# Kernel optimization log

Hardware: AMD Instinct MI355X
Metric: run time of the kernel (lower is better)

Reference implementation:

```python
import jax, jax.numpy as jnp
import numpy as np

B, S, R, D, A, P = 64, 128, 8, 10000, 10, 256


def setup_inputs() -> dict:
    key = jax.random.key(0)
    ks = jax.random.split(key, 7)
    return {
        "atom_hvs": jax.random.normal(ks[0], (A, D), jnp.float32),
        "pos_hvs": jax.random.normal(ks[1], (S, D), jnp.float32),
        "closure_tag": jax.random.normal(ks[2], (D,), jnp.float32),
        "W": jax.random.normal(ks[3], (P, D), jnp.float32) / np.float32(np.sqrt(D)),
        "b": jax.random.normal(ks[4], (P,), jnp.float32) * 0.01,
        "token_mask": jnp.ones((B, S), jnp.float32),
        "ring_mask": jnp.ones((B, R), jnp.float32),
        "atom_idx": jax.random.randint(ks[5], (B, S), 0, A),
        "ring_pos": jax.random.randint(ks[6], (B, R, 2), 0, S),
    }


def reference(atom_hvs, pos_hvs, closure_tag, W, b, token_mask, ring_mask, atom_idx, ring_pos):
    # HRR bind = circular convolution -> pointwise multiply in rFFT domain.
    # Bundle = sum; by linearity we sum in the frequency domain and do a
    # single irfft per molecule (same math as per-token conv + add).
    d = atom_hvs.shape[-1]
    Fa = jnp.fft.rfft(atom_hvs, axis=-1)          # [A, F]
    Fp = jnp.fft.rfft(pos_hvs, axis=-1)           # [S, F]
    Fc = jnp.fft.rfft(closure_tag)                # [F]

    s = atom_idx.shape[1]
    tok = Fa[atom_idx] * Fp[None, :s, :]          # [B, S, F] gather+bind
    freq = jnp.sum(token_mask[..., None] * tok, axis=1)   # [B, F] bundle

    ring = Fp[ring_pos[..., 0]] * Fp[ring_pos[..., 1]] * Fc  # [B, R, F]
    freq = freq + jnp.sum(ring_mask[..., None] * ring, axis=1)

    mol_hv = jnp.fft.irfft(freq, n=d, axis=-1)    # [B, D]
    return mol_hv @ W.T + b                       # [B, proj_dim]
```

## Files before the change

kernel.cpp:

```cpp
#include <hip/hip_runtime.h>

#define PI2 6.28318530717958647692f

#define NSIG 139
#define FS   5120

__global__ __launch_bounds__(256) void k_fwd(
                     const float* __restrict__ atom, const float* __restrict__ pos,
                     const float* __restrict__ clo, float2* __restrict__ spec) {
  __shared__ float xs[4000];
  unsigned sig = blockIdx.x, q = blockIdx.y;
  unsigned k1base = q * 10u;
  unsigned nk1 = (k1base + 10u <= 51u) ? 10u : (51u - k1base);
  const float* xb = (sig < 128u) ? (pos + sig * 10000u)
                   : ((sig < 138u) ? (atom + (sig - 128u) * 10000u) : clo);
  int tid = threadIdx.x;
  unsigned ntile1 = nk1 * 25u;
  unsigned k1l = tid / 25u, n2 = (tid % 25u) * 4u;
  bool have = (unsigned)tid < ntile1;
  unsigned k1 = k1base + k1l;
  float cth, sth;
  __sincosf(PI2 * (float)k1 * 0.01f, &sth, &cth);
  float c = 1.0f, s = 0.0f;
  float ar[4] = {}, as[4] = {};

  if (have) {
#pragma unroll 10
    for (int n1l = 0; n1l < 100; ++n1l) {
      const float4 xv = *(const float4*)(xb + n1l * 100 + n2);
      ar[0] += xv.x * c; as[0] += xv.x * s;
      ar[1] += xv.y * c; as[1] += xv.y * s;
      ar[2] += xv.z * c; as[2] += xv.z * s;
      ar[3] += xv.w * c; as[3] += xv.w * s;
      float cn = c * cth - s * sth;
      float sn = s * cth + c * sth;
      c = cn; s = sn;
    }
    unsigned rb = (100u - k1) % 100u;
    float resA[8], resB[8];
#pragma unroll
    for (int j = 0; j < 4; ++j) {
      float swA, cwA, swB, cwB;
      __sincosf(PI2 * (float)((n2 + j) * k1) * 1e-4f, &swA, &cwA);
      __sincosf(PI2 * (float)((n2 + j) * rb) * 1e-4f, &swB, &cwB);
      resA[2 * j + 0] = ar[j] * cwA - as[j] * swA;
      resA[2 * j + 1] = -(as[j] * cwA + ar[j] * swA);
      resB[2 * j + 0] = ar[j] * cwB + as[j] * swB;
      resB[2 * j + 1] = as[j] * cwB - ar[j] * swB;
    }
    float* pA = xs + k1l * 200u + n2 * 2u;
    float* pB = xs + (nk1 + k1l) * 200u + n2 * 2u;
    *(float4*)(pA + 0) = make_float4(resA[0], resA[1], resA[2], resA[3]);
    *(float4*)(pA + 4) = make_float4(resA[4], resA[5], resA[6], resA[7]);
    *(float4*)(pB + 0) = make_float4(resB[0], resB[1], resB[2], resB[3]);
    *(float4*)(pB + 4) = make_float4(resB[4], resB[5], resB[6], resB[7]);
  }
  __syncthreads();

  unsigned nrow = 2u * nk1;
  unsigned ntile3 = nrow * 26u;
  for (unsigned t = tid; t < ntile3; t += 256u) {
    unsigned lr = t / 26u, k2 = (t % 26u) * 2u;
    unsigned gk1 = (lr < nk1) ? (k1base + lr) : ((100u - (k1base + (lr - nk1))) % 100u);
    const float* brow = xs + lr * 200u;
    float cthA, sthA, cthB, sthB;
    __sincosf(PI2 * (float)k2 * 0.01f, &sthA, &cthA);
    __sincosf(PI2 * (float)(k2 + 1) * 0.01f, &sthB, &cthB);
    float cA = 1.0f, sA = 0.0f, cB = 1.0f, sB = 0.0f;
    float reA = 0.f, imA = 0.f, reB = 0.f, imB = 0.f;
#pragma unroll 4
    for (int n2i = 0; n2i < 100; n2i += 2) {
      const float4 b0 = *(const float4*)(brow + 2 * n2i);
      reA += b0.x * cA + b0.y * sA;  imA += b0.y * cA - b0.x * sA;
      reB += b0.x * cB + b0.y * sB;  imB += b0.y * cB - b0.x * sB;
      float cA1 = cA * cthA - sA * sthA, sA1 = sA * cthA + cA * sthA;
      float cB1 = cB * cthB - sB * sthB, sB1 = sB * cthB + cB * sthB;
      reA += b0.z * cA1 + b0.w * sA1;  imA += b0.w * cA1 - b0.z * sA1;
      reB += b0.z * cB1 + b0.w * sB1;  imB += b0.w * cB1 - b0.z * sB1;
      cA = cA1 * cthA - sA1 * sthA; sA = sA1 * cthA + cA1 * sthA;
      cB = cB1 * cthB - sB1 * sthB; sB = sB1 * cthB + cB1 * sthB;
    }
    unsigned kA = gk1 + 100u * k2;
    unsigned kB = gk1 + 100u * (k2 + 1);
    if (kA <= 5000u) spec[sig * FS + kA] = make_float2(reA, imA);
    if (kB <= 5000u) spec[sig * FS + kB] = make_float2(reB, imB);
  }
}

__global__ __launch_bounds__(256) void k_mix(const float2* __restrict__ spec,
                      const float* __restrict__ tmask, const float* __restrict__ rmask,
                      const int* __restrict__ aidx, const int* __restrict__ rpos,
                      float2* __restrict__ G) {
  __shared__ float2 FaS[10][128];
  __shared__ float2 FcS[128];
  __shared__ float tmS[4][128];
  __shared__ int   aiS[4][128];
  __shared__ float rmS[4][8];
  __shared__ int   rpS[4][8][2];
  __shared__ float2 red[2][4][128];
  int tid = threadIdx.x;
  int kl = tid & 127, half = tid >> 7;
  int k = blockIdx.x * 128 + kl;
  int kc = k > 5000 ? 5000 : k;
  int b0 = blockIdx.y * 4;
  for (int i = tid; i < 10 * 128; i += 256) {
    int a = i >> 7, kk = i & 127;
    int kg = blockIdx.x * 128 + kk; if (kg > 5000) kg = 5000;
    FaS[a][kk] = spec[(128 + a) * FS + kg];
  }
  if (tid < 128) FcS[tid] = spec[138 * FS + kc];
  for (int i = tid; i < 4 * 128; i += 256) {
    int bb = i >> 7, ss = i & 127;
    tmS[bb][ss] = tmask[(b0 + bb) * 128 + ss];
    aiS[bb][ss] = aidx[(b0 + bb) * 128 + ss];
  }
  if (tid < 32) {
    int bb = tid >> 3, rr = tid & 7;
    rmS[bb][rr] = rmask[(b0 + bb) * 8 + rr];
    rpS[bb][rr][0] = rpos[((b0 + bb) * 8 + rr) * 2 + 0];
    rpS[bb][rr][1] = rpos[((b0 + bb) * 8 + rr) * 2 + 1];
  }
  __syncthreads();
  float fr[4] = {}, fi[4] = {};
  int sbase = half * 64;
#pragma unroll 8
  for (int si = 0; si < 64; ++si) {
    int s = sbase + si;
    float2 fp = spec[s * FS + kc];
#pragma unroll
    for (int b = 0; b < 4; ++b) {
      int a = aiS[b][s];
      float tm = tmS[b][s];
      float2 fa = FaS[a][kl];
      fr[b] += tm * (fa.x * fp.x - fa.y * fp.y);
      fi[b] += tm * (fa.x * fp.y + fa.y * fp.x);
    }
  }
  float2 fc = FcS[kl];
#pragma unroll
  for (int rr = 0; rr < 4; ++rr) {
    int r = half * 4 + rr;
#pragma unroll
    for (int b = 0; b < 4; ++b) {
      int p0 = rpS[b][r][0], p1 = rpS[b][r][1];
      float rm = rmS[b][r];
      float2 f0 = spec[p0 * FS + kc];
      float2 f1 = spec[p1 * FS + kc];
      float tr = f0.x * f1.x - f0.y * f1.y;
      float ti = f0.x * f1.y + f0.y * f1.x;
      fr[b] += rm * (tr * fc.x - ti * fc.y);
      fi[b] += rm * (tr * fc.y + ti * fc.x);
    }
  }
#pragma unroll
  for (int b = 0; b < 4; ++b) red[half][b][kl] = make_float2(fr[b], fi[b]);
  __syncthreads();
  if (k <= 5000) {
#pragma unroll
    for (int j = 0; j < 2; ++j) {
      int b = half + 2 * j;
      float R = red[0][b][kl].x + red[1][b][kl].x;
      float I = red[0][b][kl].y + red[1][b][kl].y;
      if (k == 0 || k == 5000) I = 0.0f;
      G[(size_t)(b0 + b) * 10000 + k] = make_float2(R, I);
      if (k >= 1 && k <= 4999)
        G[(size_t)(b0 + b) * 10000 + (10000 - k)] = make_float2(R, -I);
    }
  }
}

__global__ __launch_bounds__(256) void k_i1(const float2* __restrict__ G,
                                            float2* __restrict__ Bi) {
  unsigned sig = blockIdx.x;
  const float* gp = (const float*)(G + sig * 10000u);
  int tid = threadIdx.x;
  unsigned t = blockIdx.y * 256u + tid;
  if (t >= 2600u) return;
  unsigned m1 = t / 26u, n2 = (t % 26u) * 2u;
  float cth, sth;
  __sincosf(PI2 * (float)m1 * 0.01f, &sth, &cth);
  float reA = 0.f, imA = 0.f, reB = 0.f, imB = 0.f;

  for (int h = 0; h < 4; ++h) {
    unsigned ph = (m1 * (unsigned)h) & 3u;
    float c = (ph == 0u) ? 1.0f : (ph == 2u) ? -1.0f : 0.0f;
    float s = (ph == 1u) ? 1.0f : (ph == 3u) ? -1.0f : 0.0f;
#pragma unroll 5
    for (int n1l = 0; n1l < 25; ++n1l) {
      const float4 gv = *(const float4*)(gp + (h * 25 + n1l) * 200 + n2 * 2);
      reA += gv.x * c - gv.y * s;  imA += gv.y * c + gv.x * s;
      reB += gv.z * c - gv.w * s;  imB += gv.w * c + gv.z * s;
      float cn = c * cth - s * sth;
      float sn = s * cth + c * sth;
      c = cn; s = sn;
    }
  }
  float w0 = (n2 == 0u || n2 == 50u) ? 0.5f : 1.0f;
  float w1 = (n2 == 50u) ? 0.0f : 1.0f;
  float sw0, cw0, sw1, cw1;
  __sincosf(PI2 * (float)(n2 * m1) * 1e-4f, &sw0, &cw0);
  __sincosf(PI2 * (float)((n2 + 1u) * m1) * 1e-4f, &sw1, &cw1);
  float4 outv;
  outv.x = (reA * cw0 - imA * sw0) * w0;
  outv.y = (imA * cw0 + reA * sw0) * w0;
  outv.z = (reB * cw1 - imB * sw1) * w1;
  outv.w = (imB * cw1 + reB * sw1) * w1;
  *(float4*)((float*)Bi + (sig * 5200u + m1 * 52u + n2) * 2) = outv;
}

__global__ __launch_bounds__(256) void k_i2(const float2* __restrict__ Bi,
                                            float* __restrict__ mol) {
  unsigned sig = blockIdx.x, q = blockIdx.y;
  int tid = threadIdx.x;
  unsigned t = blockIdx.z * 256u + tid;
  if (t >= 1250u) return;
  unsigned m1l = t / 50u;
  unsigned m2 = (t % 50u) * 2u;
  const float* b0 = (const float*)Bi + sig * 10400u + q * 2600u + m1l * 104u;
  float cthA, sthA, cthB, sthB;
  __sincosf(PI2 * (float)m2 * 0.01f, &sthA, &cthA);
  __sincosf(PI2 * (float)(m2 + 1u) * 0.01f, &sthB, &cthB);
  float cA = 1.0f, sA = 0.0f, cB = 1.0f, sB = 0.0f;
  float r0 = 0.f, r1 = 0.f;
#pragma unroll 4
  for (int jj = 0; jj < 26; ++jj) {
    int n2i = 2 * jj;
    const float4 v0 = *(const float4*)(b0 + 2 * n2i);
    r0 += v0.x * cA - v0.y * sA;
    r1 += v0.x * cB - v0.y * sB;
    float cA1 = cA * cthA - sA * sthA, sA1 = sA * cthA + cA * sthA;
    float cB1 = cB * cthB - sB * sthB, sB1 = sB * cthB + cB * sthB;
    r0 += v0.z * cA1 - v0.w * sA1;
    r1 += v0.z * cB1 - v0.w * sB1;
    cA = cA1 * cthA - sA1 * sthA; sA = sA1 * cthA + cA1 * sthA;
    cB = cB1 * cthB - sB1 * sthB; sB = sB1 * cthB + cB1 * sthB;
  }
  unsigned m1 = q * 25u + m1l;
  mol[sig * 10000u + m1 + 100u * m2] = r0 * 2e-4f;
  mol[sig * 10000u + m1 + 100u * (m2 + 1u)] = r1 * 2e-4f;
}

__global__ __launch_bounds__(512) void k_proj(const float* __restrict__ mol,
                                              const float* __restrict__ W,
                                              float* __restrict__ part) {
  __shared__ float molS[40 * 66];
  __shared__ float WS[40][258];
  int tid = threadIdx.x;
  int d0 = blockIdx.x * 40;
  for (int i = tid; i < 40 * 64; i += 512) {
    int b = i / 40, dl = i % 40;
    molS[dl * 66 + b] = mol[(size_t)b * 10000 + d0 + dl];
  }
  for (int i = tid; i < 40 * 256; i += 512) {
    int p = i / 40, dl = i % 40;
    WS[dl][p] = W[(size_t)p * 10000 + d0 + dl];
  }
  __syncthreads();
  int p0 = (tid & 127) * 2;
  int bh = (tid >> 7) * 16;
  float acc[2][16] = {};
#pragma unroll 4
  for (int dl = 0; dl < 40; ++dl) {
    const float2 wv = *(const float2*)(&WS[dl][p0]);
    const float2* m2p = (const float2*)(molS + dl * 66 + bh);
#pragma unroll
    for (int qq = 0; qq < 8; ++qq) {
      float2 mv = m2p[qq];
      acc[0][2 * qq + 0] += wv.x * mv.x;  acc[1][2 * qq + 0] += wv.y * mv.x;
      acc[0][2 * qq + 1] += wv.x * mv.y;  acc[1][2 * qq + 1] += wv.y * mv.y;
    }
  }
#pragma unroll
  for (int b = 0; b < 16; ++b)
    *(float2*)(part + (size_t)blockIdx.x * 16384 + (bh + b) * 256 + p0) =
        make_float2(acc[0][b], acc[1][b]);
}

__global__ __launch_bounds__(256) void k_red(const float* __restrict__ part,
                                             const float* __restrict__ bias,
                                             float* __restrict__ out) {
  __shared__ float red[4][64];
  int tid = threadIdx.x;
  int pl = tid & 63, cg = tid >> 6;
  int b = blockIdx.x;
  int p = blockIdx.y * 64 + pl;
  float acc = 0.0f;
#pragma unroll 8
  for (int ch = cg; ch < 250; ch += 4)
    acc += part[(size_t)ch * 16384 + b * 256 + p];
  red[cg][pl] = acc;
  __syncthreads();
  if (tid < 64)
    out[b * 256 + p] = red[0][pl] + red[1][pl] + red[2][pl] + red[3][pl] + bias[p];
}

extern "C" void kernel_launch(void* const* d_in, const int* in_sizes, int n_in,
                              void* d_out, int out_size, void* d_ws, size_t ws_size,
                              hipStream_t stream) {
  const float* atom  = (const float*)d_in[0];
  const float* pos   = (const float*)d_in[1];
  const float* clo   = (const float*)d_in[2];
  const float* W     = (const float*)d_in[3];
  const float* bias  = (const float*)d_in[4];
  const float* tmask = (const float*)d_in[5];
  const float* rmask = (const float*)d_in[6];
  const int*   aidx  = (const int*)d_in[7];
  const int*   rpos  = (const int*)d_in[8];
  float* out = (float*)d_out;

  char* ws = (char*)d_ws;
  size_t off = 0;
  auto alloc = [&](size_t n) { off = (off + 255) & ~(size_t)255; size_t o = off; off += n; return o; };
  char* regA   = ws + alloc(16777216);
  float2* Bi   = (float2*)regA;
  float*  part = (float*)regA;
  float2* spec = (float2*)(ws + alloc((size_t)NSIG * FS * 8));
  float2* G    = (float2*)(ws + alloc((size_t)64 * 10000 * 8));
  float*  mol  = (float*)(ws + alloc((size_t)64 * 10000 * 4));

  k_fwd<<<dim3(NSIG, 6), dim3(256), 0, stream>>>(atom, pos, clo, spec);
  k_mix<<<dim3(40, 16), dim3(256), 0, stream>>>(spec, tmask, rmask, aidx, rpos, G);
  k_i1<<<dim3(64, 11), dim3(256), 0, stream>>>(G, Bi);
  k_i2<<<dim3(64, 4, 5), dim3(256), 0, stream>>>(Bi, mol);
  k_proj<<<dim3(250), dim3(512), 0, stream>>>(mol, W, part);
  k_red<<<dim3(64, 4), dim3(256), 0, stream>>>(part, bias, out);
}
```

Baseline: 185.4 us.

## Apply radix-4 pre-butterflies in LDS to shrink DFT inner loops

In the forward and first inverse DFT stages, inputs are first combined with a radix-4 butterfly: sums and differences of the four quarter-offset elements are staged in shared memory. The per-thread twiddle loops then run over 25 terms instead of 100, picking the precombined arrays by the index modulo 4. The second forward stage gets the same treatment across its 100-point rows. This cuts multiply-adds and global reads, at the cost of extra LDS traffic, extra syncs and a larger shared-memory footprint, which may lower occupancy.

```diff
diff --git a/kernel.cpp b/kernel.cpp
--- a/kernel.cpp
+++ b/kernel.cpp
@@ -8,36 +8,75 @@
 __global__ __launch_bounds__(256) void k_fwd(
                      const float* __restrict__ atom, const float* __restrict__ pos,
                      const float* __restrict__ clo, float2* __restrict__ spec) {
-  __shared__ float xs[4000];
+  __shared__ float lds[10000];
   unsigned sig = blockIdx.x, q = blockIdx.y;
   unsigned k1base = q * 10u;
   unsigned nk1 = (k1base + 10u <= 51u) ? 10u : (51u - k1base);
   const float* xb = (sig < 128u) ? (pos + sig * 10000u)
                    : ((sig < 138u) ? (atom + (sig - 128u) * 10000u) : clo);
   int tid = threadIdx.x;
+
+  {
+    float* csA = lds;
+    float* csB = lds + 2500;
+    float* csG = lds + 5000;
+    float* csH = lds + 7500;
+    for (int t2 = tid; t2 < 625; t2 += 256) {
+      const float* p = xb + (t2 / 25) * 100 + (t2 % 25) * 4;
+      float4 x0 = *(const float4*)(p);
+      float4 x1 = *(const float4*)(p + 2500);
+      float4 x2 = *(const float4*)(p + 5000);
+      float4 x3 = *(const float4*)(p + 7500);
+      float4 A, B, G, H;
+      A.x = (x0.x + x2.x) + (x1.x + x3.x);
+      A.y = (x0.y + x2.y) + (x1.y + x3.y);
+      A.z = (x0.z + x2.z) + (x1.z + x3.z);
+      A.w = (x0.w + x2.w) + (x1.w + x3.w);
+      B.x = (x0.x + x2.x) - (x1.x + x3.x);
+      B.y = (x0.y + x2.y) - (x1.y + x3.y);
+      B.z = (x0.z + x2.z) - (x1.z + x3.z);
+      B.w = (x0.w + x2.w) - (x1.w + x3.w);
+      G.x = x0.x - x2.x;  G.y = x0.y - x2.y;
+      G.z = x0.z - x2.z;  G.w = x0.w - x2.w;
+      H.x = x1.x - x3.x;  H.y = x1.y - x3.y;
+      H.z = x1.z - x3.z;  H.w = x1.w - x3.w;
+      *(float4*)(csA + t2 * 4) = A;
+      *(float4*)(csB + t2 * 4) = B;
+      *(float4*)(csG + t2 * 4) = G;
+      *(float4*)(csH + t2 * 4) = H;
+    }
+  }
+  __syncthreads();
+
   unsigned ntile1 = nk1 * 25u;
-  unsigned k1l = tid / 25u, n2 = (tid % 25u) * 4u;
+  unsigned k1l = tid / 25u, n2q = (unsigned)tid % 25u, n2 = n2q * 4u;
   bool have = (unsigned)tid < ntile1;
   unsigned k1 = k1base + k1l;
-  float cth, sth;
-  __sincosf(PI2 * (float)k1 * 0.01f, &sth, &cth);
-  float c = 1.0f, s = 0.0f;
-  float ar[4] = {}, as[4] = {};
-
+  float resA[8], resB[8];
   if (have) {
-#pragma unroll 10
-    for (int n1l = 0; n1l < 100; ++n1l) {
-      const float4 xv = *(const float4*)(xb + n1l * 100 + n2);
-      ar[0] += xv.x * c; as[0] += xv.x * s;
-      ar[1] += xv.y * c; as[1] += xv.y * s;
-      ar[2] += xv.z * c; as[2] += xv.z * s;
-      ar[3] += xv.w * c; as[3] += xv.w * s;
+    float cth, sth;
+    __sincosf(PI2 * (float)k1 * 0.01f, &sth, &cth);
+    unsigned m = k1 & 3u;
+    const float4* creP = (const float4*)((m == 0u) ? lds
+                          : (m == 2u) ? (lds + 2500) : (lds + 5000)) + n2q;
+    const float4* cimP = (const float4*)(lds + 7500) + n2q;
+    float im_mul = (m == 1u) ? 1.0f : (m == 3u) ? -1.0f : 0.0f;
+    float c = 1.0f, s = 0.0f;
+    float ar[4] = {}, as[4] = {};
+#pragma unroll 5
+    for (int n1l = 0; n1l < 25; ++n1l) {
+      float4 Cre = creP[n1l * 25];
+      float4 Cim = cimP[n1l * 25];
+      float se = im_mul * s, ce = im_mul * c;
+      ar[0] += Cre.x * c - Cim.x * se;  as[0] += Cim.x * ce + Cre.x * s;
+      ar[1] += Cre.y * c - Cim.y * se;  as[1] += Cim.y * ce + Cre.y * s;
+      ar[2] += Cre.z * c - Cim.z * se;  as[2] += Cim.z * ce + Cre.z * s;
+      ar[3] += Cre.w * c - Cim.w * se;  as[3] += Cim.w * ce + Cre.w * s;
       float cn = c * cth - s * sth;
       float sn = s * cth + c * sth;
       c = cn; s = sn;
     }
     unsigned rb = (100u - k1) % 100u;
-    float resA[8], resB[8];
 #pragma unroll
     for (int j = 0; j < 4; ++j) {
       float swA, cwA, swB, cwB;
@@ -48,6 +87,10 @@
       resB[2 * j + 0] = ar[j] * cwB + as[j] * swB;
       resB[2 * j + 1] = as[j] * cwB - ar[j] * swB;
     }
+  }
+  __syncthreads();
+  float* xs = lds;
+  if (have) {
     float* pA = xs + k1l * 200u + n2 * 2u;
     float* pB = xs + (nk1 + k1l) * 200u + n2 * 2u;
     *(float4*)(pA + 0) = make_float4(resA[0], resA[1], resA[2], resA[3]);
@@ -58,27 +101,55 @@
   __syncthreads();
 
   unsigned nrow = 2u * nk1;
+  float* cse = lds + 4000;
+  float* cso = lds + 6000;
+  for (int t3 = tid; t3 < (int)(nrow * 25u); t3 += 256) {
+    const float* br = xs + (t3 / 25) * 200;
+    int n2l = t3 % 25;
+    float2 b0 = *(const float2*)(br + 2 * n2l);
+    float2 b1 = *(const float2*)(br + 2 * (25 + n2l));
+    float2 b2 = *(const float2*)(br + 2 * (50 + n2l));
+    float2 b3 = *(const float2*)(br + 2 * (75 + n2l));
+    float4 e, o;
+    e.x = (b0.x + b2.x) + (b1.x + b3.x);
+    e.y = (b0.y + b2.y) + (b1.y + b3.y);
+    e.z = (b0.x + b2.x) - (b1.x + b3.x);
+    e.w = (b0.y + b2.y) - (b1.y + b3.y);
+    o.x = b0.x - b2.x;
+    o.y = b1.y - b3.y;
+    o.z = b0.y - b2.y;
+    o.w = b1.x - b3.x;
+    *(float4*)(cse + t3 * 4) = e;
+    *(float4*)(cso + t3 * 4) = o;
+  }
+  __syncthreads();
+
   unsigned ntile3 = nrow * 26u;
   for (unsigned t = tid; t < ntile3; t += 256u) {
     unsigned lr = t / 26u, k2 = (t % 26u) * 2u;
     unsigned gk1 = (lr < nk1) ? (k1base + lr) : ((100u - (k1base + (lr - nk1))) % 100u);
-    const float* brow = xs + lr * 200u;
     float cthA, sthA, cthB, sthB;
     __sincosf(PI2 * (float)k2 * 0.01f, &sthA, &cthA);
     __sincosf(PI2 * (float)(k2 + 1) * 0.01f, &sthB, &cthB);
+    bool hi = (k2 & 2u) != 0u;
+    float sq = hi ? -1.0f : 1.0f;
+    const float4* pe = (const float4*)(cse + lr * 100);
+    const float4* po = (const float4*)(cso + lr * 100);
     float cA = 1.0f, sA = 0.0f, cB = 1.0f, sB = 0.0f;
     float reA = 0.f, imA = 0.f, reB = 0.f, imB = 0.f;
-#pragma unroll 4
-    for (int n2i = 0; n2i < 100; n2i += 2) {
-      const float4 b0 = *(const float4*)(brow + 2 * n2i);
-      reA += b0.x * cA + b0.y * sA;  imA += b0.y * cA - b0.x * sA;
-      reB += b0.x * cB + b0.y * sB;  imB += b0.y * cB - b0.x * sB;
+#pragma unroll 5
+    for (int n2l = 0; n2l < 25; ++n2l) {
+      float4 e = pe[n2l];
+      float4 o = po[n2l];
+      float car = hi ? e.z : e.x;
+      float cai = hi ? e.w : e.y;
+      float cbr = o.x + sq * o.y;
+      float cbi = o.z - sq * o.w;
+      reA += car * cA + cai * sA;  imA += cai * cA - car * sA;
+      reB += cbr * cB + cbi * sB;  imB += cbi * cB - cbr * sB;
       float cA1 = cA * cthA - sA * sthA, sA1 = sA * cthA + cA * sthA;
       float cB1 = cB * cthB - sB * sthB, sB1 = sB * cthB + cB * sthB;
-      reA += b0.z * cA1 + b0.w * sA1;  imA += b0.w * cA1 - b0.z * sA1;
-      reB += b0.z * cB1 + b0.w * sB1;  imB += b0.w * cB1 - b0.z * sB1;
-      cA = cA1 * cthA - sA1 * sthA; sA = sA1 * cthA + cA1 * sthA;
-      cB = cB1 * cthB - sB1 * sthB; sB = sB1 * cthB + cB1 * sthB;
+      cA = cA1; sA = sA1; cB = cB1; sB = sB1;
     }
     unsigned kA = gk1 + 100u * k2;
     unsigned kB = gk1 + 100u * (k2 + 1);
@@ -171,29 +242,63 @@
 
 __global__ __launch_bounds__(256) void k_i1(const float2* __restrict__ G,
                                             float2* __restrict__ Bi) {
+  __shared__ float lds[10400];
   unsigned sig = blockIdx.x;
   const float* gp = (const float*)(G + sig * 10000u);
   int tid = threadIdx.x;
+  float* c0v = lds;
+  float* c2v = lds + 2600;
+  float* cpr = lds + 5200;
+  float* cqt = lds + 7800;
+  for (int t2 = tid; t2 < 650; t2 += 256) {
+    const float* p = gp + (t2 / 26) * 200 + (t2 % 26) * 4;
+    float4 g0 = *(const float4*)(p);
+    float4 g1 = *(const float4*)(p + 5000);
+    float4 g2 = *(const float4*)(p + 10000);
+    float4 g3 = *(const float4*)(p + 15000);
+    float4 a, b, pr, qt;
+    a.x = (g0.x + g2.x) + (g1.x + g3.x);
+    a.y = (g0.y + g2.y) + (g1.y + g3.y);
+    a.z = (g0.z + g2.z) + (g1.z + g3.z);
+    a.w = (g0.w + g2.w) + (g1.w + g3.w);
+    b.x = (g0.x + g2.x) - (g1.x + g3.x);
+    b.y = (g0.y + g2.y) - (g1.y + g3.y);
+    b.z = (g0.z + g2.z) - (g1.z + g3.z);
+    b.w = (g0.w + g2.w) - (g1.w + g3.w);
+    pr.x = g0.x - g2.x;  pr.y = g0.y - g2.y;
+    pr.z = g0.z - g2.z;  pr.w = g0.w - g2.w;
+    qt.x = g1.y - g3.y;  qt.y = g1.x - g3.x;
+    qt.z = g1.w - g3.w;  qt.w = g1.z - g3.z;
+    *(float4*)(c0v + t2 * 4) = a;
+    *(float4*)(c2v + t2 * 4) = b;
+    *(float4*)(cpr + t2 * 4) = pr;
+    *(float4*)(cqt + t2 * 4) = qt;
+  }
+  __syncthreads();
   unsigned t = blockIdx.y * 256u + tid;
   if (t >= 2600u) return;
-  unsigned m1 = t / 26u, n2 = (t % 26u) * 2u;
+  unsigned m1 = t / 26u, n2p = t % 26u, n2 = n2p * 2u;
   float cth, sth;
   __sincosf(PI2 * (float)m1 * 0.01f, &sth, &cth);
+  unsigned m = m1 & 3u;
+  const float4* pe = (const float4*)((m == 0u) ? c0v : (m == 2u) ? c2v : cpr) + n2p;
+  const float4* pq = (const float4*)cqt + n2p;
+  float qmul = (m == 1u) ? -1.0f : (m == 3u) ? 1.0f : 0.0f;
+  float c = 1.0f, s = 0.0f;
   float reA = 0.f, imA = 0.f, reB = 0.f, imB = 0.f;
-
-  for (int h = 0; h < 4; ++h) {
-    unsigned ph = (m1 * (unsigned)h) & 3u;
-    float c = (ph == 0u) ? 1.0f : (ph == 2u) ? -1.0f : 0.0f;
-    float s = (ph == 1u) ? 1.0f : (ph == 3u) ? -1.0f : 0.0f;
 #pragma unroll 5
-    for (int n1l = 0; n1l < 25; ++n1l) {
-      const float4 gv = *(const float4*)(gp + (h * 25 + n1l) * 200 + n2 * 2);
-      reA += gv.x * c - gv.y * s;  imA += gv.y * c + gv.x * s;
-      reB += gv.z * c - gv.w * s;  imB += gv.w * c + gv.z * s;
-      float cn = c * cth - s * sth;
-      float sn = s * cth + c * sth;
-      c = cn; s = sn;
-    }
+  for (int n1l = 0; n1l < 25; ++n1l) {
+    float4 ev = pe[n1l * 26];
+    float4 qv = pq[n1l * 26];
+    float gx = ev.x + qmul * qv.x;
+    float gy = ev.y - qmul * qv.y;
+    float gz = ev.z + qmul * qv.z;
+    float gw = ev.w - qmul * qv.w;
+    reA += gx * c - gy * s;  imA += gy * c + gx * s;
+    reB += gz * c - gw * s;  imB += gw * c + gz * s;
+    float cn = c * cth - s * sth;
+    float sn = s * cth + c * sth;
+    c = cn; s = sn;
   }
   float w0 = (n2 == 0u || n2 == 50u) ? 0.5f : 1.0f;
   float w1 = (n2 == 50u) ? 0.0f : 1.0f;
```

Result: faster. 166.8 us (-10.0%).
